# Kernel optimization log

Hardware: AMD Instinct MI355X
Metric: run time of the kernel (lower is better)

Reference implementation:

```python
import jax, jax.numpy as jnp
import numpy as np

B, T, D, U = 32, 2048, 256, 512  # batch, seq_len, input_dim, enc_units


def gru_layer(x, h0, kernel, rec_kernel, bias):
    """Keras GRU (v2, reset_after=True) over a full sequence.
    x: [B,T,D_in], h0: [B,U], kernel: [D_in,3U], rec_kernel: [U,3U], bias: [2,3U].
    Returns (outputs [B,T,U], final state [B,U])."""
    b_in, b_rec = bias[0], bias[1]
    # Precompute input projections for all timesteps (the parallel part).
    xproj = jnp.einsum('btd,dk->btk', x, kernel) + b_in  # [B,T,3U]

    def step(h, xt):
        inner = h @ rec_kernel + b_rec                    # [B,3U]
        x_z, x_r, x_h = jnp.split(xt, 3, axis=-1)
        r_z, r_r, r_h = jnp.split(inner, 3, axis=-1)
        z = jax.nn.sigmoid(x_z + r_z)
        r = jax.nn.sigmoid(x_r + r_r)
        hh = jnp.tanh(x_h + r * r_h)                      # reset_after candidate
        h_new = z * h + (1.0 - z) * hh
        return h_new, h_new

    h_T, ys = jax.lax.scan(step, h0, jnp.swapaxes(xproj, 0, 1))  # time-major scan
    return jnp.swapaxes(ys, 0, 1), h_T


def setup_inputs() -> dict:
    key = jax.random.key(0)
    ks = jax.random.split(key, 8)
    def glorot(k, shape):
        lim = np.sqrt(6.0 / (shape[0] + shape[1])).astype(np.float32)
        return jax.random.uniform(k, shape, jnp.float32, -lim, lim)
    x = jax.random.normal(ks[0], (B, T, D), jnp.float32)
    hidden = jnp.zeros((B, U), jnp.float32)
    k1 = glorot(ks[1], (D, 3 * U))
    rk1 = glorot(ks[2], (U, 3 * U))
    b1 = jnp.zeros((2, 3 * U), jnp.float32)
    k2 = glorot(ks[3], (U, 3 * U))
    rk2 = glorot(ks[4], (U, 3 * U))
    b2 = jnp.zeros((2, 3 * U), jnp.float32)
    return {"x": x, "hidden": hidden, "k1": k1, "rk1": rk1, "b1": b1,
            "k2": k2, "rk2": rk2, "b2": b2}


def reference(x, hidden, k1, rk1, b1, k2, rk2, b2):
    out1, state1 = gru_layer(x, hidden, k1, rk1, b1)
    out2, state2 = gru_layer(out1, hidden, k2, rk2, b2)  # layer2 also seeded with `hidden`, per source
    return (out2, state1, state2)
```

## Files before the change

### kernel.cpp

```cpp
#include <hip/hip_runtime.h>
#include <hip/hip_bf16.h>
#include <cstdint>
#include <cstddef>

#define TSEQ 2048
#define BB   32
#define UU   512
#define NCOL 1536
#define NSB  256
#define GBLK 32

__global__ __launch_bounds__(256)
void gemm_bias(const float* __restrict__ A, const float* __restrict__ W,
               const float* __restrict__ bias, float* __restrict__ C,
               int M, int N, int K)
{
    __shared__ float As[16][68];
    __shared__ float Bs[16][64];

    const int tid = threadIdx.x;
    const int tx = tid & 15, ty = tid >> 4;
    const int m0 = blockIdx.y * 64, n0 = blockIdx.x * 64;

    float acc[4][4] = {};

    for (int k0 = 0; k0 < K; k0 += 16) {
        {
            int r  = tid >> 2;
            int kq = (tid & 3) * 4;
            float4 av = *(const float4*)&A[(size_t)(m0 + r) * K + k0 + kq];
            As[kq + 0][r] = av.x;
            As[kq + 1][r] = av.y;
            As[kq + 2][r] = av.z;
            As[kq + 3][r] = av.w;
        }
        {
            int kk = tid >> 4;
            int n  = (tid & 15) * 4;
            *(float4*)&Bs[kk][n] = *(const float4*)&W[(size_t)(k0 + kk) * N + n0 + n];
        }
        __syncthreads();

        #pragma unroll
        for (int kk = 0; kk < 16; ++kk) {
            float av0 = As[kk][ty * 4 + 0];
            float av1 = As[kk][ty * 4 + 1];
            float av2 = As[kk][ty * 4 + 2];
            float av3 = As[kk][ty * 4 + 3];
            float4 bv = *(const float4*)&Bs[kk][tx * 4];
            acc[0][0] = fmaf(av0, bv.x, acc[0][0]);
            acc[0][1] = fmaf(av0, bv.y, acc[0][1]);
            acc[0][2] = fmaf(av0, bv.z, acc[0][2]);
            acc[0][3] = fmaf(av0, bv.w, acc[0][3]);
            acc[1][0] = fmaf(av1, bv.x, acc[1][0]);
            acc[1][1] = fmaf(av1, bv.y, acc[1][1]);
            acc[1][2] = fmaf(av1, bv.z, acc[1][2]);
            acc[1][3] = fmaf(av1, bv.w, acc[1][3]);
            acc[2][0] = fmaf(av2, bv.x, acc[2][0]);
            acc[2][1] = fmaf(av2, bv.y, acc[2][1]);
            acc[2][2] = fmaf(av2, bv.z, acc[2][2]);
            acc[2][3] = fmaf(av2, bv.w, acc[2][3]);
            acc[3][0] = fmaf(av3, bv.x, acc[3][0]);
            acc[3][1] = fmaf(av3, bv.y, acc[3][1]);
            acc[3][2] = fmaf(av3, bv.z, acc[3][2]);
            acc[3][3] = fmaf(av3, bv.w, acc[3][3]);
        }
        __syncthreads();
    }

    float4 bb = *(const float4*)&bias[n0 + tx * 4];
    #pragma unroll
    for (int i = 0; i < 4; ++i) {
        float4 v;
        v.x = acc[i][0] + bb.x;
        v.y = acc[i][1] + bb.y;
        v.z = acc[i][2] + bb.z;
        v.w = acc[i][3] + bb.w;
        *(float4*)&C[(size_t)(m0 + ty * 4 + i) * N + n0 + tx * 4] = v;
    }
}

__global__ __launch_bounds__(512, 2)
void gru_scan(const float* __restrict__ xproj,
              const float* __restrict__ rk,
              const float* __restrict__ brec,
              const float* __restrict__ h0,
              float* hA, float* hB,
              int* flags,
              float* __restrict__ out,
              float* __restrict__ state_out)
{
    __shared__ __align__(16) float hl[4][512];
    __shared__ float inn[48][4];
    __shared__ float xp[2][192];

    const int tid  = threadIdx.x;
    const int bid  = blockIdx.x;
    const int g    = bid & 7;
    const int slot = bid >> 3;
    const int u0   = slot * 16;
    const int b0   = g * 4;
    const int cl   = tid >> 3;
    const int j    = tid & 7;
    const int j2   = j << 2;

    float wreg[64];
    if (cl < 48) {
        const int col = (cl >> 4) * UU + u0 + (cl & 15);
        const float* base = rk + (size_t)(j * 64) * NCOL + col;
        #pragma unroll
        for (int q = 0; q < 64; ++q) wreg[q] = base[(size_t)q * NCOL];
    }

    float brz = 0.f, brr = 0.f, brh = 0.f;
    if (tid < 64) {
        int iu = tid & 15;
        brz = brec[u0 + iu];
        brr = brec[UU + u0 + iu];
        brh = brec[2 * UU + u0 + iu];
    }

    if (tid >= 384) {
        int p = tid - 384;
        {
            int c = p >> 2, b = p & 3;
            xp[0][p] = xproj[((size_t)(b0 + b) * TSEQ + 0) * NCOL
                             + (c >> 4) * UU + u0 + (c & 15)];
        }
        int p2 = p + 128;
        if (p2 < 192) {
            int c = p2 >> 2, b = p2 & 3;
            xp[0][p2] = xproj[((size_t)(b0 + b) * TSEQ + 0) * NCOL
                              + (c >> 4) * UU + u0 + (c & 15)];
        }
    }

    for (int t = 0; t < TSEQ; ++t) {
        if (t > 0) {
            if (tid < 64) {
                int* f = flags + g * GBLK + (tid & 31);
                for (;;) {
                    int v = __hip_atomic_load(f, __ATOMIC_RELAXED,
                                              __HIP_MEMORY_SCOPE_AGENT);
                    if (__all(v >= t)) break;
                    __builtin_amdgcn_s_sleep(1);
                }
            }
        }
        __syncthreads();

        const float* hc = (t & 1) ? hA : hB;
        #pragma unroll
        for (int i = 0; i < 4; ++i) {
            int idx = i * 512 + tid;
            int row = idx >> 9, k = idx & 511;
            float v;
            if (t == 0) {
                v = h0[(size_t)(b0 + row) * UU + k];
            } else {
                v = __int_as_float(__hip_atomic_load(
                        (const int*)&hc[(size_t)(b0 + row) * UU + k],
                        __ATOMIC_RELAXED, __HIP_MEMORY_SCOPE_AGENT));
            }
            int pos = k ^ (((k >> 6) & 7) << 2);
            hl[row][pos] = v;
        }
        __syncthreads();

        if (cl < 48) {
            const int kb = j * 64;
            float a0 = 0.f, a1 = 0.f, a2 = 0.f, a3 = 0.f;
            #pragma unroll
            for (int q0 = 0; q0 < 64; q0 += 4) {
                int p = kb + (q0 ^ j2);
                float4 h0v = *(const float4*)&hl[0][p];
                float4 h1v = *(const float4*)&hl[1][p];
                float4 h2v = *(const float4*)&hl[2][p];
                float4 h3v = *(const float4*)&hl[3][p];
                a0 = fmaf(wreg[q0+0], h0v.x, a0); a1 = fmaf(wreg[q0+0], h1v.x, a1);
                a2 = fmaf(wreg[q0+0], h2v.x, a2); a3 = fmaf(wreg[q0+0], h3v.x, a3);
                a0 = fmaf(wreg[q0+1], h0v.y, a0); a1 = fmaf(wreg[q0+1], h1v.y, a1);
                a2 = fmaf(wreg[q0+1], h2v.y, a2); a3 = fmaf(wreg[q0+1], h3v.y, a3);
                a0 = fmaf(wreg[q0+2], h0v.z, a0); a1 = fmaf(wreg[q0+2], h1v.z, a1);
                a2 = fmaf(wreg[q0+2], h2v.z, a2); a3 = fmaf(wreg[q0+2], h3v.z, a3);
                a0 = fmaf(wreg[q0+3], h0v.w, a0); a1 = fmaf(wreg[q0+3], h1v.w, a1);
                a2 = fmaf(wreg[q0+3], h2v.w, a2); a3 = fmaf(wreg[q0+3], h3v.w, a3);
            }
            #pragma unroll
            for (int m = 1; m < 8; m <<= 1) {
                a0 += __shfl_xor(a0, m);
                a1 += __shfl_xor(a1, m);
                a2 += __shfl_xor(a2, m);
                a3 += __shfl_xor(a3, m);
            }
            if (j == 0) {
                inn[cl][0] = a0; inn[cl][1] = a1;
                inn[cl][2] = a2; inn[cl][3] = a3;
            }
        } else if (tid >= 384 && t + 1 < TSEQ) {
            int nb = (t + 1) & 1;
            int p = tid - 384;
            {
                int c = p >> 2, b = p & 3;
                xp[nb][p] = xproj[((size_t)(b0 + b) * TSEQ + (t + 1)) * NCOL
                                  + (c >> 4) * UU + u0 + (c & 15)];
            }
            int p2 = p + 128;
            if (p2 < 192) {
                int c = p2 >> 2, b = p2 & 3;
                xp[nb][p2] = xproj[((size_t)(b0 + b) * TSEQ + (t + 1)) * NCOL
                                   + (c >> 4) * UU + u0 + (c & 15)];
            }
        }
        __syncthreads();

        if (tid < 64) {
            int bl = tid >> 4, iu = tid & 15;
            int ug = u0 + iu;
            float iz = inn[iu][bl]      + brz;
            float ir = inn[16 + iu][bl] + brr;
            float ih = inn[32 + iu][bl] + brh;
            const float* x = xp[t & 1];
            float xz = x[iu * 4 + bl];
            float xr = x[(16 + iu) * 4 + bl];
            float xh = x[(32 + iu) * 4 + bl];
            float z  = 1.f / (1.f + expf(-(xz + iz)));
            float r  = 1.f / (1.f + expf(-(xr + ir)));
            float hh = tanhf(xh + r * ih);
            int pos = ug ^ (((ug >> 6) & 7) << 2);
            float hold = hl[bl][pos];
            float hnew = z * hold + (1.f - z) * hh;
            float* hn = (t & 1) ? hB : hA;
            __hip_atomic_store((int*)&hn[(size_t)(b0 + bl) * UU + ug],
                               __float_as_int(hnew),
                               __ATOMIC_RELAXED, __HIP_MEMORY_SCOPE_AGENT);
            out[((size_t)(b0 + bl) * TSEQ + t) * UU + ug] = hnew;
            if (t == TSEQ - 1) state_out[(size_t)(b0 + bl) * UU + ug] = hnew;
        }
        __syncthreads();
        if (tid == 0)
            __hip_atomic_store(&flags[g * GBLK + slot], t + 1,
                               __ATOMIC_RELAXED, __HIP_MEMORY_SCOPE_AGENT);
    }
}

extern "C" void kernel_launch(void* const* d_in, const int* in_sizes, int n_in,
                              void* d_out, int out_size, void* d_ws, size_t ws_size,
                              hipStream_t stream)
{
    const float* x      = (const float*)d_in[0];
    const float* hidden = (const float*)d_in[1];
    const float* k1     = (const float*)d_in[2];
    const float* rk1    = (const float*)d_in[3];
    const float* b1     = (const float*)d_in[4];
    const float* k2     = (const float*)d_in[5];
    const float* rk2    = (const float*)d_in[6];
    const float* b2     = (const float*)d_in[7];

    const int M = BB * TSEQ;
    const size_t XPROJ_ELEMS = (size_t)M * NCOL;

    float* xproj  = (float*)d_ws;
    float* hA     = xproj + XPROJ_ELEMS;
    float* hB     = hA + BB * UU;
    int*   flags1 = (int*)(hB + BB * UU);
    int*   flags2 = flags1 + NSB;

    size_t need = (XPROJ_ELEMS + 2 * (size_t)BB * UU) * sizeof(float)
                + 2 * NSB * sizeof(int);
    if (ws_size < need) return;

    float* out    = (float*)d_out;
    float* state1 = out + (size_t)BB * TSEQ * UU;
    float* state2 = state1 + BB * UU;

    hipMemsetAsync(flags1, 0, 2 * NSB * sizeof(int), stream);

    dim3 ggrid(NCOL / 64, M / 64);

    gemm_bias<<<ggrid, 256, 0, stream>>>(x, k1, b1, xproj, M, NCOL, 256);
    gru_scan<<<NSB, 512, 0, stream>>>(xproj, rk1, b1 + NCOL, hidden,
                                      hA, hB, flags1, out, state1);
    gemm_bias<<<ggrid, 256, 0, stream>>>(out, k2, b2, xproj, M, NCOL, 512);
    gru_scan<<<NSB, 512, 0, stream>>>(xproj, rk2, b2 + NCOL, hidden,
                                      hA, hB, flags2, out, state2);
}
```

Before: 18.50 ms.

## Fuse both GRU layers into one persistent wavefront-pipelined kernel

Replaces the two input-projection GEMMs and two sequential scans with a single persistent kernel. 256 blocks run layer 1 and 256 run layer 2, with layer 2 trailing layer 1 through an 8-slot ring buffer of hidden states guarded by flags. Input projections are computed per timestep from weights held in registers, with k1, k2 and rk2 stored as bf16 to fit. This removes the xproj round trip through memory and lets the two layers overlap in time. In exchange it reduces precision, puts more work on each step's critical path, and requires all 512 blocks to be co-resident or the spin-waits deadlock.

After: 55.95 ms. +202.5%, slower.

```diff
diff --git a/kernel.cpp b/kernel.cpp
--- a/kernel.cpp
+++ b/kernel.cpp
@@ -5,242 +5,313 @@
 
 #define TSEQ 2048
 #define BB   32
+#define DD   256
 #define UU   512
 #define NCOL 1536
-#define NSB  256
-#define GBLK 32
-
-__global__ __launch_bounds__(256)
-void gemm_bias(const float* __restrict__ A, const float* __restrict__ W,
-               const float* __restrict__ bias, float* __restrict__ C,
-               int M, int N, int K)
+#define GB   32
+#define RING 8
+
+static __device__ __forceinline__ float aload(const float* p) {
+    return __int_as_float(__hip_atomic_load((const int*)p, __ATOMIC_RELAXED,
+                                            __HIP_MEMORY_SCOPE_AGENT));
+}
+static __device__ __forceinline__ void astore(float* p, float v) {
+    __hip_atomic_store((int*)p, __float_as_int(v), __ATOMIC_RELAXED,
+                       __HIP_MEMORY_SCOPE_AGENT);
+}
+static __device__ __forceinline__ unsigned f2bfu(float f) {
+    __hip_bfloat16 b = __float2bfloat16(f);
+    unsigned short s;
+    __builtin_memcpy(&s, &b, 2);
+    return (unsigned)s;
+}
+static __device__ __forceinline__ float bflo(unsigned u) { return __uint_as_float(u << 16); }
+static __device__ __forceinline__ float bfhi(unsigned u) { return __uint_as_float(u & 0xffff0000u); }
+static __device__ __forceinline__ int swz512(int k) { return k ^ (((k >> 6) & 7) << 2); }
+static __device__ __forceinline__ int swz256(int k) { return k ^ (((k >> 5) & 7) << 2); }
+
+__global__ __launch_bounds__(512, 4)
+void gru_fused(const float* __restrict__ x,   const float* __restrict__ h0,
+               const float* __restrict__ k1,  const float* __restrict__ rk1,
+               const float* __restrict__ b1,  const float* __restrict__ k2,
+               const float* __restrict__ rk2, const float* __restrict__ b2,
+               float* h1ring,
+               float* hp2,
+               int* aflags, int* cflags,
+               float* __restrict__ out2, float* __restrict__ state1,
+               float* __restrict__ state2)
 {
-    __shared__ float As[16][68];
-    __shared__ float Bs[16][64];
-
-    const int tid = threadIdx.x;
-    const int tx = tid & 15, ty = tid >> 4;
-    const int m0 = blockIdx.y * 64, n0 = blockIdx.x * 64;
-
-    float acc[4][4] = {};
-
-    for (int k0 = 0; k0 < K; k0 += 16) {
-        {
-            int r  = tid >> 2;
-            int kq = (tid & 3) * 4;
-            float4 av = *(const float4*)&A[(size_t)(m0 + r) * K + k0 + kq];
-            As[kq + 0][r] = av.x;
-            As[kq + 1][r] = av.y;
-            As[kq + 2][r] = av.z;
-            As[kq + 3][r] = av.w;
-        }
-        {
-            int kk = tid >> 4;
-            int n  = (tid & 15) * 4;
-            *(float4*)&Bs[kk][n] = *(const float4*)&W[(size_t)(k0 + kk) * N + n0 + n];
-        }
-        __syncthreads();
-
-        #pragma unroll
-        for (int kk = 0; kk < 16; ++kk) {
-            float av0 = As[kk][ty * 4 + 0];
-            float av1 = As[kk][ty * 4 + 1];
-            float av2 = As[kk][ty * 4 + 2];
-            float av3 = As[kk][ty * 4 + 3];
-            float4 bv = *(const float4*)&Bs[kk][tx * 4];
-            acc[0][0] = fmaf(av0, bv.x, acc[0][0]);
-            acc[0][1] = fmaf(av0, bv.y, acc[0][1]);
-            acc[0][2] = fmaf(av0, bv.z, acc[0][2]);
-            acc[0][3] = fmaf(av0, bv.w, acc[0][3]);
-            acc[1][0] = fmaf(av1, bv.x, acc[1][0]);
-            acc[1][1] = fmaf(av1, bv.y, acc[1][1]);
-            acc[1][2] = fmaf(av1, bv.z, acc[1][2]);
-            acc[1][3] = fmaf(av1, bv.w, acc[1][3]);
-            acc[2][0] = fmaf(av2, bv.x, acc[2][0]);
-            acc[2][1] = fmaf(av2, bv.y, acc[2][1]);
-            acc[2][2] = fmaf(av2, bv.z, acc[2][2]);
-            acc[2][3] = fmaf(av2, bv.w, acc[2][3]);
-            acc[3][0] = fmaf(av3, bv.x, acc[3][0]);
-            acc[3][1] = fmaf(av3, bv.y, acc[3][1]);
-            acc[3][2] = fmaf(av3, bv.z, acc[3][2]);
-            acc[3][3] = fmaf(av3, bv.w, acc[3][3]);
-        }
-        __syncthreads();
-    }
-
-    float4 bb = *(const float4*)&bias[n0 + tx * 4];
-    #pragma unroll
-    for (int i = 0; i < 4; ++i) {
-        float4 v;
-        v.x = acc[i][0] + bb.x;
-        v.y = acc[i][1] + bb.y;
-        v.z = acc[i][2] + bb.z;
-        v.w = acc[i][3] + bb.w;
-        *(float4*)&C[(size_t)(m0 + ty * 4 + i) * N + n0 + tx * 4] = v;
-    }
-}
-
-__global__ __launch_bounds__(512, 2)
-void gru_scan(const float* __restrict__ xproj,
-              const float* __restrict__ rk,
-              const float* __restrict__ brec,
-              const float* __restrict__ h0,
-              float* hA, float* hB,
-              int* flags,
-              float* __restrict__ out,
-              float* __restrict__ state_out)
-{
-    __shared__ __align__(16) float hl[4][512];
-    __shared__ float inn[48][4];
-    __shared__ float xp[2][192];
+    __shared__ float hl1[4][512];
+    __shared__ float hl2[4][512];
+    __shared__ float xls[2][4][256];
+    __shared__ float innR[48][4];
+    __shared__ float innX[48][4];
 
     const int tid  = threadIdx.x;
     const int bid  = blockIdx.x;
-    const int g    = bid & 7;
-    const int slot = bid >> 3;
-    const int u0   = slot * 16;
-    const int b0   = g * 4;
-    const int cl   = tid >> 3;
-    const int j    = tid & 7;
-    const int j2   = j << 2;
-
-    float wreg[64];
-    if (cl < 48) {
-        const int col = (cl >> 4) * UU + u0 + (cl & 15);
-        const float* base = rk + (size_t)(j * 64) * NCOL + col;
+    const bool isA = (bid < 256);
+    const int lb   = isA ? bid : (bid - 256);
+    const int g    = lb & 7,  slot = lb >> 3;
+    const int u0   = slot * 16, b0 = g * 4;
+    const int c    = tid >> 3, j = tid & 7;
+    const int jsw  = j << 2;
+    const int col  = (c < 48) ? ((c >> 4) * UU + u0 + (c & 15)) : 0;
+
+    if (isA) {
+        float    wr[64];
+        unsigned wk[16];
+        if (c < 48) {
+            const float* rb = rk1 + (size_t)(j * 64) * NCOL + col;
+            #pragma unroll
+            for (int q = 0; q < 64; ++q) wr[q] = rb[(size_t)q * NCOL];
+            const float* kb = k1 + (size_t)(j * 32) * NCOL + col;
+            #pragma unroll
+            for (int m = 0; m < 16; ++m)
+                wk[m] = f2bfu(kb[(size_t)(2 * m) * NCOL])
+                      | (f2bfu(kb[(size_t)(2 * m + 1) * NCOL]) << 16);
+        }
+        float binz = 0, binr = 0, binh = 0, brz = 0, brr = 0, brh = 0;
+        if (tid < 64) {
+            int iu = tid & 15;
+            binz = b1[u0 + iu]; binr = b1[UU + u0 + iu]; binh = b1[2 * UU + u0 + iu];
+            brz = b1[NCOL + u0 + iu]; brr = b1[NCOL + UU + u0 + iu];
+            brh = b1[NCOL + 2 * UU + u0 + iu];
+        }
         #pragma unroll
-        for (int q = 0; q < 64; ++q) wreg[q] = base[(size_t)q * NCOL];
-    }
-
-    float brz = 0.f, brr = 0.f, brh = 0.f;
-    if (tid < 64) {
-        int iu = tid & 15;
-        brz = brec[u0 + iu];
-        brr = brec[UU + u0 + iu];
-        brh = brec[2 * UU + u0 + iu];
-    }
-
-    if (tid >= 384) {
-        int p = tid - 384;
-        {
-            int c = p >> 2, b = p & 3;
-            xp[0][p] = xproj[((size_t)(b0 + b) * TSEQ + 0) * NCOL
-                             + (c >> 4) * UU + u0 + (c & 15)];
-        }
-        int p2 = p + 128;
-        if (p2 < 192) {
-            int c = p2 >> 2, b = p2 & 3;
-            xp[0][p2] = xproj[((size_t)(b0 + b) * TSEQ + 0) * NCOL
-                              + (c >> 4) * UU + u0 + (c & 15)];
-        }
-    }
-
-    for (int t = 0; t < TSEQ; ++t) {
-        if (t > 0) {
+        for (int m = 0; m < 2; ++m) {
+            int idx = m * 512 + tid;
+            int row = idx >> 8, k = idx & 255;
+            xls[0][row][swz256(k)] = x[((size_t)(b0 + row) * TSEQ + 0) * DD + k];
+        }
+        __syncthreads();
+
+        for (int t = 0; t < TSEQ; ++t) {
+            if (t > 0) {
+                if (tid < 64) {
+                    const int* fp = (tid < 32) ? &aflags[g * GB + tid]
+                                               : &cflags[g * GB + (tid - 32)];
+                    const int thr = (tid < 32) ? t : (t - (RING - 1));
+                    while (!__all(__hip_atomic_load(fp, __ATOMIC_RELAXED,
+                                  __HIP_MEMORY_SCOPE_AGENT) >= thr)) {}
+                }
+                __syncthreads();
+            }
+            {
+                const float* hs = h1ring + (size_t)((t - 1) & 7) * BB * UU;
+                #pragma unroll
+                for (int i = 0; i < 4; ++i) {
+                    int idx = i * 512 + tid;
+                    int row = idx >> 9, k = idx & 511;
+                    float v = (t == 0) ? h0[(size_t)(b0 + row) * UU + k]
+                                       : aload(&hs[(size_t)(b0 + row) * UU + k]);
+                    hl1[row][swz512(k)] = v;
+                }
+            }
+            __syncthreads();
+
+            const int cur = t & 1;
+            if (c < 48) {
+                float aR0=0,aR1=0,aR2=0,aR3=0,aX0=0,aX1=0,aX2=0,aX3=0;
+                const int kb = j * 64;
+                #pragma unroll
+                for (int q0 = 0; q0 < 64; q0 += 4) {
+                    int p = kb + (q0 ^ jsw);
+                    float4 v0 = *(const float4*)&hl1[0][p];
+                    float4 v1 = *(const float4*)&hl1[1][p];
+                    float4 v2 = *(const float4*)&hl1[2][p];
+                    float4 v3 = *(const float4*)&hl1[3][p];
+                    aR0 = fmaf(wr[q0+0], v0.x, aR0); aR1 = fmaf(wr[q0+0], v1.x, aR1);
+                    aR2 = fmaf(wr[q0+0], v2.x, aR2); aR3 = fmaf(wr[q0+0], v3.x, aR3);
+                    aR0 = fmaf(wr[q0+1], v0.y, aR0); aR1 = fmaf(wr[q0+1], v1.y, aR1);
+                    aR2 = fmaf(wr[q0+1], v2.y, aR2); aR3 = fmaf(wr[q0+1], v3.y, aR3);
+                    aR0 = fmaf(wr[q0+2], v0.z, aR0); aR1 = fmaf(wr[q0+2], v1.z, aR1);
+                    aR2 = fmaf(wr[q0+2], v2.z, aR2); aR3 = fmaf(wr[q0+2], v3.z, aR3);
+                    aR0 = fmaf(wr[q0+3], v0.w, aR0); aR1 = fmaf(wr[q0+3], v1.w, aR1);
+                    aR2 = fmaf(wr[q0+3], v2.w, aR2); aR3 = fmaf(wr[q0+3], v3.w, aR3);
+                }
+                const int kb2 = j * 32;
+                #pragma unroll
+                for (int q0 = 0; q0 < 32; q0 += 4) {
+                    int p = kb2 + (q0 ^ jsw);
+                    float4 v0 = *(const float4*)&xls[cur][0][p];
+                    float4 v1 = *(const float4*)&xls[cur][1][p];
+                    float4 v2 = *(const float4*)&xls[cur][2][p];
+                    float4 v3 = *(const float4*)&xls[cur][3][p];
+                    unsigned wa = wk[q0 >> 1], wb = wk[(q0 >> 1) + 1];
+                    float w0 = bflo(wa), w1 = bfhi(wa), w2 = bflo(wb), w3 = bfhi(wb);
+                    aX0 = fmaf(w0, v0.x, aX0); aX1 = fmaf(w0, v1.x, aX1);
+                    aX2 = fmaf(w0, v2.x, aX2); aX3 = fmaf(w0, v3.x, aX3);
+                    aX0 = fmaf(w1, v0.y, aX0); aX1 = fmaf(w1, v1.y, aX1);
+                    aX2 = fmaf(w1, v2.y, aX2); aX3 = fmaf(w1, v3.y, aX3);
+                    aX0 = fmaf(w2, v0.z, aX0); aX1 = fmaf(w2, v1.z, aX1);
+                    aX2 = fmaf(w2, v2.z, aX2); aX3 = fmaf(w2, v3.z, aX3);
+                    aX0 = fmaf(w3, v0.w, aX0); aX1 = fmaf(w3, v1.w, aX1);
+                    aX2 = fmaf(w3, v2.w, aX2); aX3 = fmaf(w3, v3.w, aX3);
+                }
+                #pragma unroll
+                for (int m = 1; m < 8; m <<= 1) {
+                    aR0 += __shfl_xor(aR0, m); aR1 += __shfl_xor(aR1, m);
+                    aR2 += __shfl_xor(aR2, m); aR3 += __shfl_xor(aR3, m);
+                    aX0 += __shfl_xor(aX0, m); aX1 += __shfl_xor(aX1, m);
+                    aX2 += __shfl_xor(aX2, m); aX3 += __shfl_xor(aX3, m);
+                }
+                if (j == 0) {
+                    innR[c][0]=aR0; innR[c][1]=aR1; innR[c][2]=aR2; innR[c][3]=aR3;
+                    innX[c][0]=aX0; innX[c][1]=aX1; innX[c][2]=aX2; innX[c][3]=aX3;
+                }
+            } else if (t + 1 < TSEQ) {
+                int p = tid - 384, nb = (t + 1) & 1;
+                #pragma unroll
+                for (int m = 0; m < 8; ++m) {
+                    int idx = m * 128 + p;
+                    int row = idx >> 8, k = idx & 255;
+                    xls[nb][row][swz256(k)] =
+                        x[((size_t)(b0 + row) * TSEQ + (t + 1)) * DD + k];
+                }
+            }
+            __syncthreads();
+
             if (tid < 64) {
-                int* f = flags + g * GBLK + (tid & 31);
-                for (;;) {
-                    int v = __hip_atomic_load(f, __ATOMIC_RELAXED,
-                                              __HIP_MEMORY_SCOPE_AGENT);
-                    if (__all(v >= t)) break;
-                    __builtin_amdgcn_s_sleep(1);
-                }
-            }
+                int bl = tid >> 4, iu = tid & 15, ug = u0 + iu;
+                float rz = innR[iu][bl]      + brz;
+                float rr = innR[16 + iu][bl] + brr;
+                float rh = innR[32 + iu][bl] + brh;
+                float xz = innX[iu][bl]      + binz;
+                float xr = innX[16 + iu][bl] + binr;
+                float xh = innX[32 + iu][bl] + binh;
+                float z  = 1.f / (1.f + expf(-(xz + rz)));
+                float r  = 1.f / (1.f + expf(-(xr + rr)));
+                float hh = tanhf(xh + r * rh);
+                float hold = hl1[bl][swz512(ug)];
+                float hnew = z * hold + (1.f - z) * hh;
+                astore(h1ring + (size_t)(t & 7) * BB * UU
+                              + (size_t)(b0 + bl) * UU + ug, hnew);
+                if (t == TSEQ - 1) state1[(size_t)(b0 + bl) * UU + ug] = hnew;
+            }
+            __syncthreads();
+            if (tid == 0)
+                __hip_atomic_store(&aflags[g * GB + slot], t + 1,
+                                   __ATOMIC_RELAXED, __HIP_MEMORY_SCOPE_AGENT);
+        }
+    } else {
+        unsigned wr2[32];
+        unsigned wk2[32];
+        if (c < 48) {
+            const float* rb = rk2 + (size_t)(j * 64) * NCOL + col;
+            const float* kb = k2  + (size_t)(j * 64) * NCOL + col;
+            #pragma unroll
+            for (int m = 0; m < 32; ++m) {
+                wr2[m] = f2bfu(rb[(size_t)(2 * m) * NCOL])
+                       | (f2bfu(rb[(size_t)(2 * m + 1) * NCOL]) << 16);
+                wk2[m] = f2bfu(kb[(size_t)(2 * m) * NCOL])
+                       | (f2bfu(kb[(size_t)(2 * m + 1) * NCOL]) << 16);
+            }
+        }
+        float binz = 0, binr = 0, binh = 0, brz = 0, brr = 0, brh = 0;
+        if (tid < 64) {
+            int iu = tid & 15;
+            binz = b2[u0 + iu]; binr = b2[UU + u0 + iu]; binh = b2[2 * UU + u0 + iu];
+            brz = b2[NCOL + u0 + iu]; brr = b2[NCOL + UU + u0 + iu];
+            brh = b2[NCOL + 2 * UU + u0 + iu];
         }
         __syncthreads();
 
-        const float* hc = (t & 1) ? hA : hB;
-        #pragma unroll
-        for (int i = 0; i < 4; ++i) {
-            int idx = i * 512 + tid;
-            int row = idx >> 9, k = idx & 511;
-            float v;
-            if (t == 0) {
-                v = h0[(size_t)(b0 + row) * UU + k];
-            } else {
-                v = __int_as_float(__hip_atomic_load(
-                        (const int*)&hc[(size_t)(b0 + row) * UU + k],
-                        __ATOMIC_RELAXED, __HIP_MEMORY_SCOPE_AGENT));
-            }
-            int pos = k ^ (((k >> 6) & 7) << 2);
-            hl[row][pos] = v;
-        }
-        __syncthreads();
-
-        if (cl < 48) {
-            const int kb = j * 64;
-            float a0 = 0.f, a1 = 0.f, a2 = 0.f, a3 = 0.f;
-            #pragma unroll
-            for (int q0 = 0; q0 < 64; q0 += 4) {
-                int p = kb + (q0 ^ j2);
-                float4 h0v = *(const float4*)&hl[0][p];
-                float4 h1v = *(const float4*)&hl[1][p];
-                float4 h2v = *(const float4*)&hl[2][p];
-                float4 h3v = *(const float4*)&hl[3][p];
-                a0 = fmaf(wreg[q0+0], h0v.x, a0); a1 = fmaf(wreg[q0+0], h1v.x, a1);
-                a2 = fmaf(wreg[q0+0], h2v.x, a2); a3 = fmaf(wreg[q0+0], h3v.x, a3);
-                a0 = fmaf(wreg[q0+1], h0v.y, a0); a1 = fmaf(wreg[q0+1], h1v.y, a1);
-                a2 = fmaf(wreg[q0+1], h2v.y, a2); a3 = fmaf(wreg[q0+1], h3v.y, a3);
-                a0 = fmaf(wreg[q0+2], h0v.z, a0); a1 = fmaf(wreg[q0+2], h1v.z, a1);
-                a2 = fmaf(wreg[q0+2], h2v.z, a2); a3 = fmaf(wreg[q0+2], h3v.z, a3);
-                a0 = fmaf(wreg[q0+3], h0v.w, a0); a1 = fmaf(wreg[q0+3], h1v.w, a1);
-                a2 = fmaf(wreg[q0+3], h2v.w, a2); a3 = fmaf(wreg[q0+3], h3v.w, a3);
-            }
-            #pragma unroll
-            for (int m = 1; m < 8; m <<= 1) {
-                a0 += __shfl_xor(a0, m);
-                a1 += __shfl_xor(a1, m);
-                a2 += __shfl_xor(a2, m);
-                a3 += __shfl_xor(a3, m);
-            }
-            if (j == 0) {
-                inn[cl][0] = a0; inn[cl][1] = a1;
-                inn[cl][2] = a2; inn[cl][3] = a3;
-            }
-        } else if (tid >= 384 && t + 1 < TSEQ) {
-            int nb = (t + 1) & 1;
-            int p = tid - 384;
+        for (int t = 0; t < TSEQ; ++t) {
+            if (tid < 64) {
+                const int* fp = (tid < 32) ? &cflags[g * GB + tid]
+                                           : &aflags[g * GB + (tid - 32)];
+                const int thr = (tid < 32) ? t : (t + 1);
+                while (!__all(__hip_atomic_load(fp, __ATOMIC_RELAXED,
+                              __HIP_MEMORY_SCOPE_AGENT) >= thr)) {}
+            }
+            __syncthreads();
             {
-                int c = p >> 2, b = p & 3;
-                xp[nb][p] = xproj[((size_t)(b0 + b) * TSEQ + (t + 1)) * NCOL
-                                  + (c >> 4) * UU + u0 + (c & 15)];
-            }
-            int p2 = p + 128;
-            if (p2 < 192) {
-                int c = p2 >> 2, b = p2 & 3;
-                xp[nb][p2] = xproj[((size_t)(b0 + b) * TSEQ + (t + 1)) * NCOL
-                                   + (c >> 4) * UU + u0 + (c & 15)];
-            }
-        }
-        __syncthreads();
-
-        if (tid < 64) {
-            int bl = tid >> 4, iu = tid & 15;
-            int ug = u0 + iu;
-            float iz = inn[iu][bl]      + brz;
-            float ir = inn[16 + iu][bl] + brr;
-            float ih = inn[32 + iu][bl] + brh;
-            const float* x = xp[t & 1];
-            float xz = x[iu * 4 + bl];
-            float xr = x[(16 + iu) * 4 + bl];
-            float xh = x[(32 + iu) * 4 + bl];
-            float z  = 1.f / (1.f + expf(-(xz + iz)));
-            float r  = 1.f / (1.f + expf(-(xr + ir)));
-            float hh = tanhf(xh + r * ih);
-            int pos = ug ^ (((ug >> 6) & 7) << 2);
-            float hold = hl[bl][pos];
-            float hnew = z * hold + (1.f - z) * hh;
-            float* hn = (t & 1) ? hB : hA;
-            __hip_atomic_store((int*)&hn[(size_t)(b0 + bl) * UU + ug],
-                               __float_as_int(hnew),
-                               __ATOMIC_RELAXED, __HIP_MEMORY_SCOPE_AGENT);
-            out[((size_t)(b0 + bl) * TSEQ + t) * UU + ug] = hnew;
-            if (t == TSEQ - 1) state_out[(size_t)(b0 + bl) * UU + ug] = hnew;
-        }
-        __syncthreads();
-        if (tid == 0)
-            __hip_atomic_store(&flags[g * GBLK + slot], t + 1,
-                               __ATOMIC_RELAXED, __HIP_MEMORY_SCOPE_AGENT);
+                const float* hs1 = h1ring + (size_t)(t & 7) * BB * UU;
+                const float* hs2 = hp2 + (size_t)((t + 1) & 1) * BB * UU;
+                #pragma unroll
+                for (int i = 0; i < 4; ++i) {
+                    int idx = i * 512 + tid;
+                    int row = idx >> 9, k = idx & 511;
+                    hl1[row][swz512(k)] = aload(&hs1[(size_t)(b0 + row) * UU + k]);
+                    float v = (t == 0) ? h0[(size_t)(b0 + row) * UU + k]
+                                       : aload(&hs2[(size_t)(b0 + row) * UU + k]);
+                    hl2[row][swz512(k)] = v;
+                }
+            }
+            __syncthreads();
+
+            if (c < 48) {
+                float aR0=0,aR1=0,aR2=0,aR3=0,aX0=0,aX1=0,aX2=0,aX3=0;
+                const int kb = j * 64;
+                #pragma unroll
+                for (int q0 = 0; q0 < 64; q0 += 4) {
+                    int p = kb + (q0 ^ jsw);
+                    float4 v0 = *(const float4*)&hl2[0][p];
+                    float4 v1 = *(const float4*)&hl2[1][p];
+                    float4 v2 = *(const float4*)&hl2[2][p];
+                    float4 v3 = *(const float4*)&hl2[3][p];
+                    unsigned wa = wr2[q0 >> 1], wb = wr2[(q0 >> 1) + 1];
+                    float w0 = bflo(wa), w1 = bfhi(wa), w2 = bflo(wb), w3 = bfhi(wb);
+                    aR0 = fmaf(w0, v0.x, aR0); aR1 = fmaf(w0, v1.x, aR1);
+                    aR2 = fmaf(w0, v2.x, aR2); aR3 = fmaf(w0, v3.x, aR3);
+                    aR0 = fmaf(w1, v0.y, aR0); aR1 = fmaf(w1, v1.y, aR1);
+                    aR2 = fmaf(w1, v2.y, aR2); aR3 = fmaf(w1, v3.y, aR3);
+                    aR0 = fmaf(w2, v0.z, aR0); aR1 = fmaf(w2, v1.z, aR1);
+                    aR2 = fmaf(w2, v2.z, aR2); aR3 = fmaf(w2, v3.z, aR3);
+                    aR0 = fmaf(w3, v0.w, aR0); aR1 = fmaf(w3, v1.w, aR1);
+                    aR2 = fmaf(w3, v2.w, aR2); aR3 = fmaf(w3, v3.w, aR3);
+                    float4 u0v = *(const float4*)&hl1[0][p];
+                    float4 u1v = *(const float4*)&hl1[1][p];
+                    float4 u2v = *(const float4*)&hl1[2][p];
+                    float4 u3v = *(const float4*)&hl1[3][p];
+                    unsigned xa = wk2[q0 >> 1], xb = wk2[(q0 >> 1) + 1];
+                    float y0 = bflo(xa), y1 = bfhi(xa), y2 = bflo(xb), y3 = bfhi(xb);
+                    aX0 = fmaf(y0, u0v.x, aX0); aX1 = fmaf(y0, u1v.x, aX1);
+                    aX2 = fmaf(y0, u2v.x, aX2); aX3 = fmaf(y0, u3v.x, aX3);
+                    aX0 = fmaf(y1, u0v.y, aX0); aX1 = fmaf(y1, u1v.y, aX1);
+                    aX2 = fmaf(y1, u2v.y, aX2); aX3 = fmaf(y1, u3v.y, aX3);
+                    aX0 = fmaf(y2, u0v.z, aX0); aX1 = fmaf(y2, u1v.z, aX1);
+                    aX2 = fmaf(y2, u2v.z, aX2); aX3 = fmaf(y2, u3v.z, aX3);
+                    aX0 = fmaf(y3, u0v.w, aX0); aX1 = fmaf(y3, u1v.w, aX1);
+                    aX2 = fmaf(y3, u2v.w, aX2); aX3 = fmaf(y3, u3v.w, aX3);
+                }
+                #pragma unroll
+                for (int m = 1; m < 8; m <<= 1) {
+                    aR0 += __shfl_xor(aR0, m); aR1 += __shfl_xor(aR1, m);
+                    aR2 += __shfl_xor(aR2, m); aR3 += __shfl_xor(aR3, m);
+                    aX0 += __shfl_xor(aX0, m); aX1 += __shfl_xor(aX1, m);
+                    aX2 += __shfl_xor(aX2, m); aX3 += __shfl_xor(aX3, m);
+                }
+                if (j == 0) {
+                    innR[c][0]=aR0; innR[c][1]=aR1; innR[c][2]=aR2; innR[c][3]=aR3;
+                    innX[c][0]=aX0; innX[c][1]=aX1; innX[c][2]=aX2; innX[c][3]=aX3;
+                }
+            }
+            __syncthreads();
+
+            if (tid < 64) {
+                int bl = tid >> 4, iu = tid & 15, ug = u0 + iu;
+                float rz = innR[iu][bl]      + brz;
+                float rr = innR[16 + iu][bl] + brr;
+                float rh = innR[32 + iu][bl] + brh;
+                float xz = innX[iu][bl]      + binz;
+                float xr = innX[16 + iu][bl] + binr;
+                float xh = innX[32 + iu][bl] + binh;
+                float z  = 1.f / (1.f + expf(-(xz + rz)));
+                float r  = 1.f / (1.f + expf(-(xr + rr)));
+                float hh = tanhf(xh + r * rh);
+                float hold = hl2[bl][swz512(ug)];
+                float hnew = z * hold + (1.f - z) * hh;
+                astore(hp2 + (size_t)(t & 1) * BB * UU
+                           + (size_t)(b0 + bl) * UU + ug, hnew);
+                out2[((size_t)(b0 + bl) * TSEQ + t) * UU + ug] = hnew;
+                if (t == TSEQ - 1) state2[(size_t)(b0 + bl) * UU + ug] = hnew;
+            }
+            __syncthreads();
+            if (tid == 0)
+                __hip_atomic_store(&cflags[g * GB + slot], t + 1,
+                                   __ATOMIC_RELAXED, __HIP_MEMORY_SCOPE_AGENT);
+        }
     }
 }
 
@@ -257,31 +328,21 @@
     const float* rk2    = (const float*)d_in[6];
     const float* b2     = (const float*)d_in[7];
 
-    const int M = BB * TSEQ;
-    const size_t XPROJ_ELEMS = (size_t)M * NCOL;
-
-    float* xproj  = (float*)d_ws;
-    float* hA     = xproj + XPROJ_ELEMS;
-    float* hB     = hA + BB * UU;
-    int*   flags1 = (int*)(hB + BB * UU);
-    int*   flags2 = flags1 + NSB;
-
-    size_t need = (XPROJ_ELEMS + 2 * (size_t)BB * UU) * sizeof(float)
-                + 2 * NSB * sizeof(int);
+    float* h1ring = (float*)d_ws;
+    float* hp2    = h1ring + (size_t)RING * BB * UU;
+    int*   aflags = (int*)(hp2 + 2 * (size_t)BB * UU);
+    int*   cflags = aflags + 256;
+
+    size_t need = ((size_t)(RING + 2) * BB * UU) * sizeof(float) + 512 * sizeof(int);
     if (ws_size < need) return;
 
-    float* out    = (float*)d_out;
-    float* state1 = out + (size_t)BB * TSEQ * UU;
+    float* out2   = (float*)d_out;
+    float* state1 = out2 + (size_t)BB * TSEQ * UU;
     float* state2 = state1 + BB * UU;
 
-    hipMemsetAsync(flags1, 0, 2 * NSB * sizeof(int), stream);
-
-    dim3 ggrid(NCOL / 64, M / 64);
-
-    gemm_bias<<<ggrid, 256, 0, stream>>>(x, k1, b1, xproj, M, NCOL, 256);
-    gru_scan<<<NSB, 512, 0, stream>>>(xproj, rk1, b1 + NCOL, hidden,
-                                      hA, hB, flags1, out, state1);
-    gemm_bias<<<ggrid, 256, 0, stream>>>(out, k2, b2, xproj, M, NCOL, 512);
-    gru_scan<<<NSB, 512, 0, stream>>>(xproj, rk2, b2 + NCOL, hidden,
-                                      hA, hB, flags2, out, state2);
-}
+    hipMemsetAsync(aflags, 0, 512 * sizeof(int), stream);
+
+    gru_fused<<<512, 512, 0, stream>>>(x, hidden, k1, rk1, b1, k2, rk2, b2,
+                                       h1ring, hp2, aflags, cflags,
+                                       out2, state1, state2);
+}
```
